# Performance work log

Measured on AMD Instinct MI355X. Metric: run time of the kernel, lower is better.

The kernel has to match this reference:

```python
import jax, jax.numpy as jnp
import numpy as np

NEG_SLOPE = 0.2  # PyG GATConv default negative_slope
EPS = 1e-16


def gat_conv(x, src, dst, num_nodes, W, a_src, a_dst, bias, heads, out_c, concat):
    """PyG-style GATConv (eval mode, self-loops already appended).
    x: [N, F_in]; src/dst: [E] (edge j->i with src=j, dst=i).
    W: [F_in, heads*out_c]; a_src/a_dst: [heads, out_c]; bias: [heads*out_c] or [out_c].
    """
    xw = (x @ W).reshape(num_nodes, heads, out_c)          # [N, H, C]
    alpha_src = jnp.sum(xw * a_src, axis=-1)               # [N, H]
    alpha_dst = jnp.sum(xw * a_dst, axis=-1)               # [N, H]
    e = jax.nn.leaky_relu(alpha_src[src] + alpha_dst[dst], NEG_SLOPE)  # [E, H]
    # numerically stable segment softmax over edges grouped by destination node
    m = jax.ops.segment_max(e, dst, num_segments=num_nodes)            # [N, H]
    e = jnp.exp(e - m[dst])
    denom = jax.ops.segment_sum(e, dst, num_segments=num_nodes)        # [N, H]
    alpha = e / (denom[dst] + EPS)                                     # [E, H]
    # weighted scatter-sum aggregation of source messages
    out = jax.ops.segment_sum(xw[src] * alpha[:, :, None], dst, num_segments=num_nodes)  # [N, H, C]
    if concat:
        out = out.reshape(num_nodes, heads * out_c)
    else:
        out = out.mean(axis=1)
    return out + bias


def setup_inputs() -> dict:
    key = jax.random.key(0)
    ks = jax.random.split(key, 12)
    N, E = 50000, 800000
    F_in, Hid, H1, Out = 512, 32, 8, 64

    def xavier(k, shape, gain=1.414):
        fan_in, fan_out = shape[0], shape[-1] if len(shape) == 2 else int(np.prod(shape[1:]))
        a = gain * np.sqrt(6.0 / (fan_in + fan_out))
        return jax.random.uniform(k, shape, jnp.float32, -a, a)

    x = jax.random.normal(ks[0], (N, F_in), jnp.float32)
    edge_index = jax.random.randint(ks[1], (2, E), 0, N, jnp.int64)

    W1 = xavier(ks[2], (F_in, H1 * Hid))
    a_src1 = xavier(ks[3], (H1, Hid))
    a_dst1 = xavier(ks[4], (H1, Hid))
    b1 = jnp.zeros((H1 * Hid,), jnp.float32)

    W2 = xavier(ks[5], (H1 * Hid, Out))
    a_src2 = xavier(ks[6], (1, Out))
    a_dst2 = xavier(ks[7], (1, Out))
    b2 = jnp.zeros((Out,), jnp.float32)

    return {"x": x, "edge_index": edge_index,
            "W1": W1, "a_src1": a_src1, "a_dst1": a_dst1, "b1": b1,
            "W2": W2, "a_src2": a_src2, "a_dst2": a_dst2, "b2": b2}


def reference(x, edge_index, W1, a_src1, a_dst1, b1, W2, a_src2, a_dst2, b2):
    N = x.shape[0]
    # add self-loops (PyG GATConv default add_self_loops=True)
    loop = jnp.arange(N, dtype=edge_index.dtype)
    src = jnp.concatenate([edge_index[0], loop])
    dst = jnp.concatenate([edge_index[1], loop])

    # eval mode: all dropouts are identity
    h = gat_conv(x, src, dst, N, W1, a_src1, a_dst1, b1, heads=8, out_c=32, concat=True)
    h = jax.nn.elu(h)
    h = gat_conv(h, src, dst, N, W2, a_src2, a_dst2, b2, heads=1, out_c=64, concat=False)
    return jax.nn.log_softmax(h, axis=1)
```

## Files before the change

kernel.cpp:

```cpp
#include <hip/hip_runtime.h>
#include <hip/hip_bf16.h>


typedef __attribute__((ext_vector_type(8)))  __bf16          bf16x8;
typedef __attribute__((ext_vector_type(8)))  unsigned short  ushort8;
typedef __attribute__((ext_vector_type(16))) float           f32x16;

#define NEG_SLOPE 0.2f
#define EPS_GAT 1e-16f

static __device__ __forceinline__ float lrelu(float x) {
    return x > 0.0f ? x : NEG_SLOPE * x;
}
static __device__ __forceinline__ unsigned short f2bf(float f) {
    unsigned u = __float_as_uint(f);
    return (unsigned short)((u + 0x7fffu + ((u >> 16) & 1u)) >> 16);
}
static __device__ __forceinline__ float bf2f(unsigned short v) {
    return __uint_as_float(((unsigned)v) << 16);
}
static __device__ __forceinline__ unsigned encf(float x) {
    unsigned u = __float_as_uint(x);
    return (u >> 31) ? ~u : (u | 0x80000000u);
}
static __device__ __forceinline__ float decf(unsigned e) {
    unsigned u = (e >> 31) ? (e & 0x7fffffffu) : ~e;
    return __uint_as_float(u);
}

__global__ void k_flag(const unsigned* __restrict__ p, unsigned* sentinel, int E) {
    __shared__ int anynz;
    if (threadIdx.x == 0) anynz = 0;
    __syncthreads();
    int i = threadIdx.x;
    unsigned w = (i < E) ? p[2 * i + 1] : 0u;
    if (w != 0u) atomicOr(&anynz, 1);
    __syncthreads();
    if (threadIdx.x == 0 && anynz) *sentinel = 1u;
}

__global__ void k_convert(const void* __restrict__ p, const unsigned* __restrict__ sentinel,
                          int* __restrict__ esrc, int* __restrict__ edst,
                          int* __restrict__ counts, int E) {
    int i = blockIdx.x * 256 + threadIdx.x;
    if (i >= 2 * E) return;
    bool is64 = (*sentinel == 0u);
    int v = is64 ? (int)((const long long*)p)[i] : ((const int*)p)[i];
    if (i < E) {
        esrc[i] = v;
    } else {
        edst[i - E] = v;
        atomicAdd(&counts[v], 1);
    }
}

__global__ void k_scan1(const int* __restrict__ counts, int* __restrict__ rowp,
                        int* __restrict__ bsum, int N) {
    __shared__ int s[256];
    int t = threadIdx.x, i = blockIdx.x * 256 + t;
    int v = (i < N) ? counts[i] : 0;
    s[t] = v;
    __syncthreads();
    for (int off = 1; off < 256; off <<= 1) {
        int u = (t >= off) ? s[t - off] : 0;
        __syncthreads();
        s[t] += u;
        __syncthreads();
    }
    if (i < N) rowp[i] = s[t] - v;
    if (t == 255) bsum[blockIdx.x] = s[255];
}

__global__ void k_scan2(const int* __restrict__ bsum, int* __restrict__ boff,
                        int* __restrict__ rowp_last, int NB) {
    __shared__ int s[256];
    int t = threadIdx.x;
    int v = (t < NB) ? bsum[t] : 0;
    s[t] = v;
    __syncthreads();
    for (int off = 1; off < 256; off <<= 1) {
        int u = (t >= off) ? s[t - off] : 0;
        __syncthreads();
        s[t] += u;
        __syncthreads();
    }
    if (t < NB) boff[t] = s[t] - v;
    if (t == 255) *rowp_last = s[255];
}

__global__ void k_scan3(int* __restrict__ rowp, int* __restrict__ cursor,
                        const int* __restrict__ boff, int N) {
    int i = blockIdx.x * 256 + threadIdx.x;
    if (i < N) {
        int r = rowp[i] + boff[blockIdx.x];
        rowp[i] = r;
        cursor[i] = r;
    }
}

__global__ void k_fill(const int* __restrict__ esrc, const int* __restrict__ edst,
                       int* __restrict__ cursor, int* __restrict__ sorted_src, int E) {
    int i = blockIdx.x * 256 + threadIdx.x;
    if (i >= E) return;
    int d = edst[i];
    int pos = atomicAdd(&cursor[d], 1);
    sorted_src[pos] = esrc[i];
}

__global__ void k_prep_w(const float* __restrict__ W1, const float* __restrict__ W2,
                         unsigned short* __restrict__ w1t, unsigned short* __restrict__ w2t) {
    int t = blockIdx.x * 256 + threadIdx.x;
    if (t < 512 * 256) {
        int k = t >> 8, m = t & 255;
        w1t[m * 512 + k] = f2bf(W1[t]);
    } else {
        int u = t - 512 * 256;
        if (u < 256 * 64) {
            int k = u >> 6, m = u & 63;
            w2t[m * 256 + k] = f2bf(W2[u]);
        }
    }
}

template <int BM, int BN, int NT, bool AF32, bool OUTBF>
__global__ __launch_bounds__(NT) void k_gemm(const void* __restrict__ Ain,
                                             const unsigned short* __restrict__ Bt,
                                             void* __restrict__ Cout, int Nrows, int K) {
    constexpr int LD = 40;
    __shared__ __align__(16) unsigned short As[BM * LD];
    __shared__ __align__(16) unsigned short Bs[BN * LD];
    const int tid = threadIdx.x;
    const int blockRow = blockIdx.x * BM;
    const int wave = tid >> 6, lane = tid & 63;
    constexpr int WR = BM / 64;
    const int wr = wave % WR, wc = wave / WR;
    const int m = lane & 31;
    const int ksel = (lane >> 5) * 8;

    f32x16 acc00{}, acc01{}, acc10{}, acc11{};

    for (int kt = 0; kt < K; kt += 32) {
        if constexpr (AF32) {
            const float* A = (const float*)Ain;
            for (int idx = tid; idx < BM * 4; idx += NT) {
                int r = idx >> 2, kc = (idx & 3) * 8;
                int grow = blockRow + r;
                union { ushort8 u; __hip_bfloat162 h[4]; } cv;
                if (grow < Nrows) {
                    const float* ap = A + (size_t)grow * K + kt + kc;
                    float4 x0 = *(const float4*)ap;
                    float4 x1 = *(const float4*)(ap + 4);
                    cv.h[0] = __float22bfloat162_rn(make_float2(x0.x, x0.y));
                    cv.h[1] = __float22bfloat162_rn(make_float2(x0.z, x0.w));
                    cv.h[2] = __float22bfloat162_rn(make_float2(x1.x, x1.y));
                    cv.h[3] = __float22bfloat162_rn(make_float2(x1.z, x1.w));
                } else {
                    cv.u = ushort8{};
                }
                *(ushort8*)&As[r * LD + kc] = cv.u;
            }
        } else {
            const unsigned short* A = (const unsigned short*)Ain;
            for (int idx = tid; idx < BM * 4; idx += NT) {
                int r = idx >> 2, kc = (idx & 3) * 8;
                int grow = blockRow + r;
                ushort8 o{};
                if (grow < Nrows) o = *(const ushort8*)(A + (size_t)grow * K + kt + kc);
                *(ushort8*)&As[r * LD + kc] = o;
            }
        }
        for (int idx = tid; idx < BN * 4; idx += NT) {
            int r = idx >> 2, kc = (idx & 3) * 8;
            *(ushort8*)&Bs[r * LD + kc] = *(const ushort8*)(Bt + (size_t)r * K + kt + kc);
        }
        __syncthreads();

        #pragma unroll
        for (int kk = 0; kk < 32; kk += 16) {
            bf16x8 a0 = *(const bf16x8*)&As[(wr * 64 +      m) * LD + kk + ksel];
            bf16x8 a1 = *(const bf16x8*)&As[(wr * 64 + 32 + m) * LD + kk + ksel];
            bf16x8 b0 = *(const bf16x8*)&Bs[(wc * 64 +      m) * LD + kk + ksel];
            bf16x8 b1 = *(const bf16x8*)&Bs[(wc * 64 + 32 + m) * LD + kk + ksel];
            acc00 = __builtin_amdgcn_mfma_f32_32x32x16_bf16(a0, b0, acc00, 0, 0, 0);
            acc01 = __builtin_amdgcn_mfma_f32_32x32x16_bf16(a0, b1, acc01, 0, 0, 0);
            acc10 = __builtin_amdgcn_mfma_f32_32x32x16_bf16(a1, b0, acc10, 0, 0, 0);
            acc11 = __builtin_amdgcn_mfma_f32_32x32x16_bf16(a1, b1, acc11, 0, 0, 0);
        }
        __syncthreads();
    }

    const int dcol = wc * 64 + (lane & 31);
    const int dquad = 4 * (lane >> 5);
    auto store_tile = [&](const f32x16& a, int rt, int ct) {
        #pragma unroll
        for (int r = 0; r < 16; ++r) {
            int row = blockRow + wr * 64 + rt * 32 + (r & 3) + 8 * (r >> 2) + dquad;
            if (row < Nrows) {
                size_t off = (size_t)row * BN + dcol + ct * 32;
                if constexpr (OUTBF) ((unsigned short*)Cout)[off] = f2bf(a[r]);
                else                 ((float*)Cout)[off] = a[r];
            }
        }
    };
    store_tile(acc00, 0, 0); store_tile(acc01, 0, 1);
    store_tile(acc10, 1, 0); store_tile(acc11, 1, 1);
}

__global__ void k_alpha(const unsigned short* __restrict__ xw, const float* __restrict__ a_s,
                        const float* __restrict__ a_d, float* __restrict__ os,
                        float* __restrict__ od, unsigned* __restrict__ Menc,
                        int NH, int H, int C) {
    __shared__ float red[256];
    int t = blockIdx.x * 256 + threadIdx.x;
    float s = -1e30f, d = 0.f;
    if (t < NH) {
        int n = t / H, h = t - n * H;
        const unsigned short* row = xw + (size_t)n * H * C + h * C;
        s = 0.f;
        for (int c = 0; c < C; c += 8) {
            ushort8 v = *(const ushort8*)(row + c);
            #pragma unroll
            for (int q = 0; q < 8; ++q) {
                float f = bf2f(v[q]);
                s += f * a_s[h * C + c + q];
                d += f * a_d[h * C + c + q];
            }
        }
        os[t] = s; od[t] = d;
    }
    red[threadIdx.x] = s;
    __syncthreads();
    for (int off = 128; off >= H; off >>= 1) {
        if (threadIdx.x < off) red[threadIdx.x] = fmaxf(red[threadIdx.x], red[threadIdx.x + off]);
        __syncthreads();
    }
    if ((int)threadIdx.x < H) atomicMax(&Menc[threadIdx.x], encf(red[threadIdx.x]));
}

__global__ __launch_bounds__(256) void k_agg_l1(
        const unsigned short* __restrict__ xw1, const float* __restrict__ asrc,
        const float* __restrict__ adst, const unsigned* __restrict__ Menc,
        const float* __restrict__ b1, const int* __restrict__ rp,
        const int* __restrict__ ssrc, unsigned short* __restrict__ hbf, int N) {
    int wid = (blockIdx.x * 256 + threadIdx.x) >> 6;
    if (wid >= N) return;
    int lane = threadIdx.x & 63;
    int g  = lane >> 4;
    int q  = lane & 15;
    int f0 = q * 16;
    int h  = q >> 1;
    int ih = wid * 8 + h;
    float ad = adst[ih];
    float m  = lrelu(decf(Menc[h]) + ad);
    float acc[16];
    float s;
    {
        float w = (g == 0) ? __expf(lrelu(asrc[ih] + ad) - m) : 0.0f;
        const unsigned short* rowp_ = xw1 + (size_t)wid * 256 + f0;
        ushort8 lo = *(const ushort8*)rowp_;
        ushort8 hi = *(const ushort8*)(rowp_ + 8);
        s = w;
        #pragma unroll
        for (int i = 0; i < 8; ++i) { acc[i] = w * bf2f(lo[i]); acc[8 + i] = w * bf2f(hi[i]); }
    }
    int e0 = rp[wid], e1 = rp[wid + 1];
    if (e0 < e1) {
        auto loadSlot = [&](int ebase, float& as, ushort8& lo, ushort8& hi, bool& val) {
            int ei = ebase + g;
            val = ei < e1;
            int j = ssrc[val ? ei : e1 - 1];
            as = asrc[j * 8 + h];
            const unsigned short* rp_ = xw1 + (size_t)j * 256 + f0;
            lo = *(const ushort8*)rp_;
            hi = *(const ushort8*)(rp_ + 8);
        };
        float asA; ushort8 loA, hiA; bool vA;
        loadSlot(e0, asA, loA, hiA, vA);
        float asB = 0.f; ushort8 loB{}, hiB{}; bool vB = false;
        bool moreB = e0 + 4 < e1;
        if (moreB) loadSlot(e0 + 4, asB, loB, hiB, vB);
        for (int e = e0;;) {
            float asC = 0.f; ushort8 loC{}, hiC{}; bool vC = false;
            bool moreC = e + 8 < e1;
            if (moreC) loadSlot(e + 8, asC, loC, hiC, vC);
            float w = vA ? __expf(lrelu(asA + ad) - m) : 0.0f;
            s += w;
            #pragma unroll
            for (int i = 0; i < 8; ++i) {
                acc[i]     += w * bf2f(loA[i]);
                acc[8 + i] += w * bf2f(hiA[i]);
            }
            if (!moreB) break;
            asA = asB; loA = loB; hiA = hiB; vA = vB;
            asB = asC; loB = loC; hiB = hiC; vB = vC;
            moreB = moreC;
            e += 4;
        }
    }
    s += __shfl_xor(s, 16, 64);
    s += __shfl_xor(s, 32, 64);
    #pragma unroll
    for (int i = 0; i < 16; ++i) {
        acc[i] += __shfl_xor(acc[i], 16, 64);
        acc[i] += __shfl_xor(acc[i], 32, 64);
    }
    float inv = 1.0f / (s + EPS_GAT);
    int fw = f0 + g * 4;
    ushort4 o;
    #pragma unroll
    for (int i = 0; i < 4; ++i) {
        float v = acc[g * 4 + i] * inv + b1[fw + i];
        v = v > 0.f ? v : expm1f(v);
        ((unsigned short*)&o)[i] = f2bf(v);
    }
    *(ushort4*)(hbf + (size_t)wid * 256 + fw) = o;
}

__global__ __launch_bounds__(256) void k_agg_l2(
        const unsigned short* __restrict__ xw2, const float* __restrict__ asrc,
        const float* __restrict__ adst, const unsigned* __restrict__ Menc,
        const float* __restrict__ b2, const int* __restrict__ rp,
        const int* __restrict__ ssrc, float* __restrict__ out, int N) {
    int wid = (blockIdx.x * 256 + threadIdx.x) >> 6;
    if (wid >= N) return;
    int lane = threadIdx.x & 63;
    int g  = lane >> 4;
    int q  = lane & 15;
    int f0 = q * 4;
    float ad = adst[wid];
    float m = lrelu(decf(Menc[0]) + ad);
    float acc[4];
    float s;
    {
        float w = (g == 0) ? __expf(lrelu(asrc[wid] + ad) - m) : 0.0f;
        ushort4 xv = *(const ushort4*)(xw2 + (size_t)wid * 64 + f0);
        s = w;
        acc[0] = w * bf2f(xv.x); acc[1] = w * bf2f(xv.y);
        acc[2] = w * bf2f(xv.z); acc[3] = w * bf2f(xv.w);
    }
    int e0 = rp[wid], e1 = rp[wid + 1];
    if (e0 < e1) {
        auto loadSlot = [&](int ebase, float& as, ushort4& xv, bool& val) {
            int ei = ebase + g;
            val = ei < e1;
            int j = ssrc[val ? ei : e1 - 1];
            as = asrc[j];
            xv = *(const ushort4*)(xw2 + (size_t)j * 64 + f0);
        };
        float asA; ushort4 xvA; bool vA;
        loadSlot(e0, asA, xvA, vA);
        float asB = 0.f; ushort4 xvB = {0, 0, 0, 0}; bool vB = false;
        bool moreB = e0 + 4 < e1;
        if (moreB) loadSlot(e0 + 4, asB, xvB, vB);
        for (int e = e0;;) {
            float asC = 0.f; ushort4 xvC = {0, 0, 0, 0}; bool vC = false;
            bool moreC = e + 8 < e1;
            if (moreC) loadSlot(e + 8, asC, xvC, vC);
            float w = vA ? __expf(lrelu(asA + ad) - m) : 0.0f;
            s += w;
            acc[0] += w * bf2f(xvA.x); acc[1] += w * bf2f(xvA.y);
            acc[2] += w * bf2f(xvA.z); acc[3] += w * bf2f(xvA.w);
            if (!moreB) break;
            asA = asB; xvA = xvB; vA = vB;
            asB = asC; xvB = xvC; vB = vC;
            moreB = moreC;
            e += 4;
        }
    }
    s += __shfl_xor(s, 16, 64);
    s += __shfl_xor(s, 32, 64);
    #pragma unroll
    for (int i = 0; i < 4; ++i) {
        acc[i] += __shfl_xor(acc[i], 16, 64);
        acc[i] += __shfl_xor(acc[i], 32, 64);
    }
    float inv = 1.0f / (s + EPS_GAT);
    float val[4];
    float mx = -1e30f;
    #pragma unroll
    for (int i = 0; i < 4; ++i) {
        val[i] = acc[i] * inv + b2[f0 + i];
        mx = fmaxf(mx, val[i]);
    }
    #pragma unroll
    for (int off = 8; off > 0; off >>= 1) mx = fmaxf(mx, __shfl_xor(mx, off, 64));
    float sm = 0.f;
    #pragma unroll
    for (int i = 0; i < 4; ++i) sm += __expf(val[i] - mx);
    #pragma unroll
    for (int off = 8; off > 0; off >>= 1) sm += __shfl_xor(sm, off, 64);
    float lse = mx + logf(sm);
    if (g == 0) {
        float4 o = make_float4(val[0] - lse, val[1] - lse, val[2] - lse, val[3] - lse);
        *(float4*)(out + (size_t)wid * 64 + f0) = o;
    }
}

static inline int cdiv(int a, int b) { return (a + b - 1) / b; }

extern "C" void kernel_launch(void* const* d_in, const int* in_sizes, int n_in,
                              void* d_out, int out_size, void* d_ws, size_t ws_size,
                              hipStream_t stream) {
    const float* x   = (const float*)d_in[0];
    const void*  eix = d_in[1];
    const float* W1  = (const float*)d_in[2];
    const float* as1 = (const float*)d_in[3];
    const float* ad1 = (const float*)d_in[4];
    const float* b1  = (const float*)d_in[5];
    const float* W2  = (const float*)d_in[6];
    const float* as2 = (const float*)d_in[7];
    const float* ad2 = (const float*)d_in[8];
    const float* b2  = (const float*)d_in[9];
    float* out = (float*)d_out;

    const int N = in_sizes[0] / 512;
    const int E = in_sizes[1] / 2;
    const int NB = cdiv(N, 256);
    const int NB1 = cdiv(N * 8, 256);
    const int NB2 = cdiv(N, 256);
    (void)n_in; (void)out_size; (void)ws_size;

    char* base = (char*)d_ws;
    size_t o = 0;
    auto alloc = [&](size_t bytes) -> char* {
        o = (o + 255) & ~(size_t)255;
        char* p = base + o;
        o += bytes;
        return p;
    };
    unsigned short* xw1b  = (unsigned short*)alloc((size_t)N * 256 * 2);
    unsigned short* hbf   = (unsigned short*)alloc((size_t)N * 256 * 2);
    unsigned short* xw2b  = (unsigned short*)alloc((size_t)N * 64 * 2);
    float*          asrc1 = (float*)alloc((size_t)N * 8 * 4);
    float*          adst1 = (float*)alloc((size_t)N * 8 * 4);
    float*          asrc2 = (float*)alloc((size_t)N * 4);
    float*          adst2 = (float*)alloc((size_t)N * 4);
    unsigned*       Menc  = (unsigned*)alloc(16 * 4);
    unsigned short* w1t   = (unsigned short*)alloc(512 * 256 * 2);
    unsigned short* w2t   = (unsigned short*)alloc(256 * 64 * 2);
    int*            counts= (int*)alloc((size_t)N * 4);
    int*            cursor= (int*)alloc((size_t)N * 4);
    int*            rowp  = (int*)alloc((size_t)(N + 1) * 4);
    int*            bsum  = (int*)alloc(256 * 4);
    int*            boff  = (int*)alloc(256 * 4);
    int*            esrc  = (int*)alloc((size_t)E * 4);
    int*            edst  = (int*)alloc((size_t)E * 4);
    int*            ssrc  = (int*)alloc((size_t)E * 4);
    unsigned*       sent  = (unsigned*)alloc(256);

    hipMemsetAsync(sent, 0, 4, stream);
    hipMemsetAsync(Menc, 0, 16 * 4, stream);
    hipMemsetAsync(counts, 0, (size_t)N * 4, stream);

    k_flag<<<1, 256, 0, stream>>>((const unsigned*)eix, sent, E);
    k_convert<<<cdiv(2 * E, 256), 256, 0, stream>>>(eix, sent, esrc, edst, counts, E);
    k_scan1<<<NB, 256, 0, stream>>>(counts, rowp, bsum, N);
    k_scan2<<<1, 256, 0, stream>>>(bsum, boff, rowp + N, NB);
    k_scan3<<<NB, 256, 0, stream>>>(rowp, cursor, boff, N);
    k_fill<<<cdiv(E, 256), 256, 0, stream>>>(esrc, edst, cursor, ssrc, E);

    k_prep_w<<<cdiv(512 * 256 + 256 * 64, 256), 256, 0, stream>>>(W1, W2, w1t, w2t);

    k_gemm<128, 256, 512, true, true><<<cdiv(N, 128), 512, 0, stream>>>(x, w1t, xw1b, N, 512);
    k_alpha<<<NB1, 256, 0, stream>>>(xw1b, as1, ad1, asrc1, adst1, Menc, N * 8, 8, 32);
    k_agg_l1<<<cdiv(N * 64, 256), 256, 0, stream>>>(xw1b, asrc1, adst1, Menc, b1,
                                                    rowp, ssrc, hbf, N);
    k_gemm<256, 64, 256, false, true><<<cdiv(N, 256), 256, 0, stream>>>(hbf, w2t, xw2b, N, 256);
    k_alpha<<<NB2, 256, 0, stream>>>(xw2b, as2, ad2, asrc2, adst2, Menc + 8, N, 1, 64);
    k_agg_l2<<<cdiv(N * 64, 256), 256, 0, stream>>>(xw2b, asrc2, adst2, Menc + 8, b2,
                                                    rowp, ssrc, out, N);
}
```

Measured before the change: 438.5 us.

## Fuse CSR build kernels, single-block scan, and widen layer-2 aggregation lanes

Merges the int64 detection, histogram and weight-conversion into one kernel. It replaces the three-kernel scan with a single 1024-thread block scan and has the fill kernel read the edge index directly, removing the esrc/edst intermediates and two memsets. The aggregation loops now prefetch source indices two steps ahead and feature rows one step ahead. Layer 2 uses 8 edge groups of 8 features each instead of 4×16. This cuts launch count and memory traffic in preprocessing, but the single-block serial scan may be slow for N=50k.

```diff
diff --git a/kernel.cpp b/kernel.cpp
--- a/kernel.cpp
+++ b/kernel.cpp
@@ -28,98 +28,78 @@
     return __uint_as_float(u);
 }
 
-__global__ void k_flag(const unsigned* __restrict__ p, unsigned* sentinel, int E) {
-    __shared__ int anynz;
-    if (threadIdx.x == 0) anynz = 0;
+__global__ void k_hist_w(const void* __restrict__ eix, int* __restrict__ counts,
+                         int E, int EB,
+                         const float* __restrict__ W1, const float* __restrict__ W2,
+                         unsigned short* __restrict__ w1t, unsigned short* __restrict__ w2t) {
+    int b = blockIdx.x;
+    if (b < EB) {
+        int i = b * 256 + threadIdx.x;
+        unsigned w = ((const unsigned*)eix)[2 * min(i, E - 1) + 1];
+        bool is64 = (__syncthreads_or((int)(w != 0u)) == 0);
+        if (i < E) {
+            int d = is64 ? (int)((const long long*)eix)[E + i]
+                         : ((const int*)eix)[E + i];
+            atomicAdd(&counts[d], 1);
+        }
+    } else {
+        int t = (b - EB) * 256 + threadIdx.x;
+        if (t < 512 * 256) {
+            int k = t >> 8, m = t & 255;
+            w1t[m * 512 + k] = f2bf(W1[t]);
+        } else {
+            int u = t - 512 * 256;
+            if (u < 256 * 64) {
+                int k = u >> 6, m = u & 63;
+                w2t[m * 256 + k] = f2bf(W2[u]);
+            }
+        }
+    }
+}
+
+__global__ __launch_bounds__(1024) void k_scan(const int* __restrict__ counts,
+                                               int* __restrict__ rowp,
+                                               int* __restrict__ cursor, int N) {
+    __shared__ int sums[1024];
+    int tid = threadIdx.x;
+    int chunk = (N + 1023) >> 10;
+    int b = tid * chunk;
+    int e = b + chunk; if (e > N) e = N;
+    int s = 0;
+    for (int i = b; i < e; ++i) s += counts[i];
+    sums[tid] = s;
     __syncthreads();
-    int i = threadIdx.x;
-    unsigned w = (i < E) ? p[2 * i + 1] : 0u;
-    if (w != 0u) atomicOr(&anynz, 1);
-    __syncthreads();
-    if (threadIdx.x == 0 && anynz) *sentinel = 1u;
-}
-
-__global__ void k_convert(const void* __restrict__ p, const unsigned* __restrict__ sentinel,
-                          int* __restrict__ esrc, int* __restrict__ edst,
-                          int* __restrict__ counts, int E) {
+    for (int off = 1; off < 1024; off <<= 1) {
+        int v = (tid >= off) ? sums[tid - off] : 0;
+        __syncthreads();
+        sums[tid] += v;
+        __syncthreads();
+    }
+    int run = (tid > 0) ? sums[tid - 1] : 0;
+    for (int i = b; i < e; ++i) {
+        rowp[i] = run;
+        cursor[i] = run;
+        run += counts[i];
+    }
+    if (tid == 1023) rowp[N] = sums[1023];
+}
+
+__global__ void k_fill(const void* __restrict__ eix, int* __restrict__ cursor,
+                       int* __restrict__ ssrc, int E) {
     int i = blockIdx.x * 256 + threadIdx.x;
-    if (i >= 2 * E) return;
-    bool is64 = (*sentinel == 0u);
-    int v = is64 ? (int)((const long long*)p)[i] : ((const int*)p)[i];
-    if (i < E) {
-        esrc[i] = v;
+    unsigned w = ((const unsigned*)eix)[2 * min(i, E - 1) + 1];
+    bool is64 = (__syncthreads_or((int)(w != 0u)) == 0);
+    if (i >= E) return;
+    int s, d;
+    if (is64) {
+        s = (int)((const long long*)eix)[i];
+        d = (int)((const long long*)eix)[E + i];
     } else {
-        edst[i - E] = v;
-        atomicAdd(&counts[v], 1);
-    }
-}
-
-__global__ void k_scan1(const int* __restrict__ counts, int* __restrict__ rowp,
-                        int* __restrict__ bsum, int N) {
-    __shared__ int s[256];
-    int t = threadIdx.x, i = blockIdx.x * 256 + t;
-    int v = (i < N) ? counts[i] : 0;
-    s[t] = v;
-    __syncthreads();
-    for (int off = 1; off < 256; off <<= 1) {
-        int u = (t >= off) ? s[t - off] : 0;
-        __syncthreads();
-        s[t] += u;
-        __syncthreads();
-    }
-    if (i < N) rowp[i] = s[t] - v;
-    if (t == 255) bsum[blockIdx.x] = s[255];
-}
-
-__global__ void k_scan2(const int* __restrict__ bsum, int* __restrict__ boff,
-                        int* __restrict__ rowp_last, int NB) {
-    __shared__ int s[256];
-    int t = threadIdx.x;
-    int v = (t < NB) ? bsum[t] : 0;
-    s[t] = v;
-    __syncthreads();
-    for (int off = 1; off < 256; off <<= 1) {
-        int u = (t >= off) ? s[t - off] : 0;
-        __syncthreads();
-        s[t] += u;
-        __syncthreads();
-    }
-    if (t < NB) boff[t] = s[t] - v;
-    if (t == 255) *rowp_last = s[255];
-}
-
-__global__ void k_scan3(int* __restrict__ rowp, int* __restrict__ cursor,
-                        const int* __restrict__ boff, int N) {
-    int i = blockIdx.x * 256 + threadIdx.x;
-    if (i < N) {
-        int r = rowp[i] + boff[blockIdx.x];
-        rowp[i] = r;
-        cursor[i] = r;
-    }
-}
-
-__global__ void k_fill(const int* __restrict__ esrc, const int* __restrict__ edst,
-                       int* __restrict__ cursor, int* __restrict__ sorted_src, int E) {
-    int i = blockIdx.x * 256 + threadIdx.x;
-    if (i >= E) return;
-    int d = edst[i];
+        s = ((const int*)eix)[i];
+        d = ((const int*)eix)[E + i];
+    }
     int pos = atomicAdd(&cursor[d], 1);
-    sorted_src[pos] = esrc[i];
-}
-
-__global__ void k_prep_w(const float* __restrict__ W1, const float* __restrict__ W2,
-                         unsigned short* __restrict__ w1t, unsigned short* __restrict__ w2t) {
-    int t = blockIdx.x * 256 + threadIdx.x;
-    if (t < 512 * 256) {
-        int k = t >> 8, m = t & 255;
-        w1t[m * 512 + k] = f2bf(W1[t]);
-    } else {
-        int u = t - 512 * 256;
-        if (u < 256 * 64) {
-            int k = u >> 6, m = u & 63;
-            w2t[m * 256 + k] = f2bf(W2[u]);
-        }
-    }
+    ssrc[pos] = s;
 }
 
 template <int BM, int BN, int NT, bool AF32, bool OUTBF>
@@ -256,33 +236,38 @@
     float s;
     {
         float w = (g == 0) ? __expf(lrelu(asrc[ih] + ad) - m) : 0.0f;
-        const unsigned short* rowp_ = xw1 + (size_t)wid * 256 + f0;
-        ushort8 lo = *(const ushort8*)rowp_;
-        ushort8 hi = *(const ushort8*)(rowp_ + 8);
+        const unsigned short* pr = xw1 + (size_t)wid * 256 + f0;
+        ushort8 lo = *(const ushort8*)pr;
+        ushort8 hi = *(const ushort8*)(pr + 8);
         s = w;
         #pragma unroll
         for (int i = 0; i < 8; ++i) { acc[i] = w * bf2f(lo[i]); acc[8 + i] = w * bf2f(hi[i]); }
     }
     int e0 = rp[wid], e1 = rp[wid + 1];
     if (e0 < e1) {
-        auto loadSlot = [&](int ebase, float& as, ushort8& lo, ushort8& hi, bool& val) {
-            int ei = ebase + g;
-            val = ei < e1;
-            int j = ssrc[val ? ei : e1 - 1];
-            as = asrc[j * 8 + h];
-            const unsigned short* rp_ = xw1 + (size_t)j * 256 + f0;
-            lo = *(const ushort8*)rp_;
-            hi = *(const ushort8*)(rp_ + 8);
-        };
-        float asA; ushort8 loA, hiA; bool vA;
-        loadSlot(e0, asA, loA, hiA, vA);
-        float asB = 0.f; ushort8 loB{}, hiB{}; bool vB = false;
-        bool moreB = e0 + 4 < e1;
-        if (moreB) loadSlot(e0 + 4, asB, loB, hiB, vB);
-        for (int e = e0;;) {
-            float asC = 0.f; ushort8 loC{}, hiC{}; bool vC = false;
-            bool moreC = e + 8 < e1;
-            if (moreC) loadSlot(e + 8, asC, loC, hiC, vC);
+        int eA = e0;
+        bool vA = eA + g < e1;
+        int jA = ssrc[min(eA + g, e1 - 1)];
+        float asA = asrc[jA * 8 + h];
+        const unsigned short* pA = xw1 + (size_t)jA * 256 + f0;
+        ushort8 loA = *(const ushort8*)pA;
+        ushort8 hiA = *(const ushort8*)(pA + 8);
+        int eB = e0 + 4;
+        bool hasB = eB < e1;
+        bool vB = false; int jB = 0;
+        if (hasB) { vB = eB + g < e1; jB = ssrc[min(eB + g, e1 - 1)]; }
+        int eC = e0 + 8;
+        while (true) {
+            bool hasC = eC < e1;
+            bool vC = false; int jC = 0;
+            if (hasC) { vC = eC + g < e1; jC = ssrc[min(eC + g, e1 - 1)]; }
+            float asB = 0.f; ushort8 loB{}, hiB{};
+            if (hasB) {
+                asB = asrc[jB * 8 + h];
+                const unsigned short* pB = xw1 + (size_t)jB * 256 + f0;
+                loB = *(const ushort8*)pB;
+                hiB = *(const ushort8*)(pB + 8);
+            }
             float w = vA ? __expf(lrelu(asA + ad) - m) : 0.0f;
             s += w;
             #pragma unroll
@@ -290,11 +275,10 @@
                 acc[i]     += w * bf2f(loA[i]);
                 acc[8 + i] += w * bf2f(hiA[i]);
             }
-            if (!moreB) break;
-            asA = asB; loA = loB; hiA = hiB; vA = vB;
-            asB = asC; loB = loC; hiB = hiC; vB = vC;
-            moreB = moreC;
-            e += 4;
+            if (!hasB) break;
+            vA = vB; asA = asB; loA = loB; hiA = hiB;
+            jB = jC; vB = vC; hasB = hasC;
+            eC += 4;
         }
     }
     s += __shfl_xor(s, 16, 64);
@@ -324,75 +308,81 @@
     int wid = (blockIdx.x * 256 + threadIdx.x) >> 6;
     if (wid >= N) return;
     int lane = threadIdx.x & 63;
-    int g  = lane >> 4;
-    int q  = lane & 15;
-    int f0 = q * 4;
+    int g  = lane >> 3;
+    int q  = lane & 7;
+    int f0 = q * 8;
     float ad = adst[wid];
     float m = lrelu(decf(Menc[0]) + ad);
-    float acc[4];
+    float acc[8];
     float s;
     {
         float w = (g == 0) ? __expf(lrelu(asrc[wid] + ad) - m) : 0.0f;
-        ushort4 xv = *(const ushort4*)(xw2 + (size_t)wid * 64 + f0);
+        ushort8 xv = *(const ushort8*)(xw2 + (size_t)wid * 64 + f0);
         s = w;
-        acc[0] = w * bf2f(xv.x); acc[1] = w * bf2f(xv.y);
-        acc[2] = w * bf2f(xv.z); acc[3] = w * bf2f(xv.w);
+        #pragma unroll
+        for (int i = 0; i < 8; ++i) acc[i] = w * bf2f(xv[i]);
     }
     int e0 = rp[wid], e1 = rp[wid + 1];
     if (e0 < e1) {
-        auto loadSlot = [&](int ebase, float& as, ushort4& xv, bool& val) {
-            int ei = ebase + g;
-            val = ei < e1;
-            int j = ssrc[val ? ei : e1 - 1];
-            as = asrc[j];
-            xv = *(const ushort4*)(xw2 + (size_t)j * 64 + f0);
-        };
-        float asA; ushort4 xvA; bool vA;
-        loadSlot(e0, asA, xvA, vA);
-        float asB = 0.f; ushort4 xvB = {0, 0, 0, 0}; bool vB = false;
-        bool moreB = e0 + 4 < e1;
-        if (moreB) loadSlot(e0 + 4, asB, xvB, vB);
-        for (int e = e0;;) {
-            float asC = 0.f; ushort4 xvC = {0, 0, 0, 0}; bool vC = false;
-            bool moreC = e + 8 < e1;
-            if (moreC) loadSlot(e + 8, asC, xvC, vC);
+        int eA = e0;
+        bool vA = eA + g < e1;
+        int jA = ssrc[min(eA + g, e1 - 1)];
+        float asA = asrc[jA];
+        ushort8 xvA = *(const ushort8*)(xw2 + (size_t)jA * 64 + f0);
+        int eB = e0 + 8;
+        bool hasB = eB < e1;
+        bool vB = false; int jB = 0;
+        if (hasB) { vB = eB + g < e1; jB = ssrc[min(eB + g, e1 - 1)]; }
+        int eC = e0 + 16;
+        while (true) {
+            bool hasC = eC < e1;
+            bool vC = false; int jC = 0;
+            if (hasC) { vC = eC + g < e1; jC = ssrc[min(eC + g, e1 - 1)]; }
+            float asB = 0.f; ushort8 xvB{};
+            if (hasB) {
+                asB = asrc[jB];
+                xvB = *(const ushort8*)(xw2 + (size_t)jB * 64 + f0);
+            }
             float w = vA ? __expf(lrelu(asA + ad) - m) : 0.0f;
             s += w;
-            acc[0] += w * bf2f(xvA.x); acc[1] += w * bf2f(xvA.y);
-            acc[2] += w * bf2f(xvA.z); acc[3] += w * bf2f(xvA.w);
-            if (!moreB) break;
-            asA = asB; xvA = xvB; vA = vB;
-            asB = asC; xvB = xvC; vB = vC;
-            moreB = moreC;
-            e += 4;
-        }
-    }
+            #pragma unroll
+            for (int i = 0; i < 8; ++i) acc[i] += w * bf2f(xvA[i]);
+            if (!hasB) break;
+            vA = vB; asA = asB; xvA = xvB;
+            jB = jC; vB = vC; hasB = hasC;
+            eC += 8;
+        }
+    }
+    s += __shfl_xor(s, 8, 64);
     s += __shfl_xor(s, 16, 64);
     s += __shfl_xor(s, 32, 64);
     #pragma unroll
-    for (int i = 0; i < 4; ++i) {
+    for (int i = 0; i < 8; ++i) {
+        acc[i] += __shfl_xor(acc[i], 8, 64);
         acc[i] += __shfl_xor(acc[i], 16, 64);
         acc[i] += __shfl_xor(acc[i], 32, 64);
     }
     float inv = 1.0f / (s + EPS_GAT);
-    float val[4];
+    float val[8];
     float mx = -1e30f;
     #pragma unroll
-    for (int i = 0; i < 4; ++i) {
+    for (int i = 0; i < 8; ++i) {
         val[i] = acc[i] * inv + b2[f0 + i];
         mx = fmaxf(mx, val[i]);
     }
     #pragma unroll
-    for (int off = 8; off > 0; off >>= 1) mx = fmaxf(mx, __shfl_xor(mx, off, 64));
+    for (int off = 4; off > 0; off >>= 1) mx = fmaxf(mx, __shfl_xor(mx, off, 64));
     float sm = 0.f;
     #pragma unroll
-    for (int i = 0; i < 4; ++i) sm += __expf(val[i] - mx);
-    #pragma unroll
-    for (int off = 8; off > 0; off >>= 1) sm += __shfl_xor(sm, off, 64);
+    for (int i = 0; i < 8; ++i) sm += __expf(val[i] - mx);
+    #pragma unroll
+    for (int off = 4; off > 0; off >>= 1) sm += __shfl_xor(sm, off, 64);
     float lse = mx + logf(sm);
     if (g == 0) {
-        float4 o = make_float4(val[0] - lse, val[1] - lse, val[2] - lse, val[3] - lse);
-        *(float4*)(out + (size_t)wid * 64 + f0) = o;
+        float4 o0 = make_float4(val[0] - lse, val[1] - lse, val[2] - lse, val[3] - lse);
+        float4 o1 = make_float4(val[4] - lse, val[5] - lse, val[6] - lse, val[7] - lse);
+        *(float4*)(out + (size_t)wid * 64 + f0)     = o0;
+        *(float4*)(out + (size_t)wid * 64 + f0 + 4) = o1;
     }
 }
 
@@ -415,7 +405,8 @@
 
     const int N = in_sizes[0] / 512;
     const int E = in_sizes[1] / 2;
-    const int NB = cdiv(N, 256);
+    const int EB = cdiv(E, 256);
+    const int WB = cdiv(512 * 256 + 256 * 64, 256);
     const int NB1 = cdiv(N * 8, 256);
     const int NB2 = cdiv(N, 256);
     (void)n_in; (void)out_size; (void)ws_size;
@@ -435,31 +426,21 @@
     float*          adst1 = (float*)alloc((size_t)N * 8 * 4);
     float*          asrc2 = (float*)alloc((size_t)N * 4);
     float*          adst2 = (float*)alloc((size_t)N * 4);
+    size_t zero_begin = (o + 255) & ~(size_t)255;
     unsigned*       Menc  = (unsigned*)alloc(16 * 4);
+    int*            counts= (int*)alloc((size_t)N * 4);
+    size_t zero_end = o;
+    int*            cursor= (int*)alloc((size_t)N * 4);
+    int*            rowp  = (int*)alloc((size_t)(N + 1) * 4);
     unsigned short* w1t   = (unsigned short*)alloc(512 * 256 * 2);
     unsigned short* w2t   = (unsigned short*)alloc(256 * 64 * 2);
-    int*            counts= (int*)alloc((size_t)N * 4);
-    int*            cursor= (int*)alloc((size_t)N * 4);
-    int*            rowp  = (int*)alloc((size_t)(N + 1) * 4);
-    int*            bsum  = (int*)alloc(256 * 4);
-    int*            boff  = (int*)alloc(256 * 4);
-    int*            esrc  = (int*)alloc((size_t)E * 4);
-    int*            edst  = (int*)alloc((size_t)E * 4);
     int*            ssrc  = (int*)alloc((size_t)E * 4);
-    unsigned*       sent  = (unsigned*)alloc(256);
-
-    hipMemsetAsync(sent, 0, 4, stream);
-    hipMemsetAsync(Menc, 0, 16 * 4, stream);
-    hipMemsetAsync(counts, 0, (size_t)N * 4, stream);
-
-    k_flag<<<1, 256, 0, stream>>>((const unsigned*)eix, sent, E);
-    k_convert<<<cdiv(2 * E, 256), 256, 0, stream>>>(eix, sent, esrc, edst, counts, E);
-    k_scan1<<<NB, 256, 0, stream>>>(counts, rowp, bsum, N);
-    k_scan2<<<1, 256, 0, stream>>>(bsum, boff, rowp + N, NB);
-    k_scan3<<<NB, 256, 0, stream>>>(rowp, cursor, boff, N);
-    k_fill<<<cdiv(E, 256), 256, 0, stream>>>(esrc, edst, cursor, ssrc, E);
-
-    k_prep_w<<<cdiv(512 * 256 + 256 * 64, 256), 256, 0, stream>>>(W1, W2, w1t, w2t);
+
+    hipMemsetAsync(base + zero_begin, 0, zero_end - zero_begin, stream);
+
+    k_hist_w<<<EB + WB, 256, 0, stream>>>(eix, counts, E, EB, W1, W2, w1t, w2t);
+    k_scan<<<1, 1024, 0, stream>>>(counts, rowp, cursor, N);
+    k_fill<<<EB, 256, 0, stream>>>(eix, cursor, ssrc, E);
 
     k_gemm<128, 256, 512, true, true><<<cdiv(N, 128), 512, 0, stream>>>(x, w1t, xw1b, N, 512);
     k_alpha<<<NB1, 256, 0, stream>>>(xw1b, as1, ad1, asrc1, adst1, Menc, N * 8, 8, 32);
```

Result: slower. 526.8 us (+20.2%).
